# Kernel optimization log

Measured on AMD Instinct MI355X. Metric: run time of the kernel, lower is better.

Reference implementation:

```python
import jax, jax.numpy as jnp
import numpy as np
from jax import lax

TAU = 20.0
DT = 1.0
THRESH = 1.0

# Hard-threshold spike with surrogate gradient (triangular window around thresh),
# matching torch SpikeFunction.
@jax.custom_vjp
def spike(v):
    return (v >= THRESH).astype(v.dtype)

def _spike_fwd(v):
    return spike(v), v

def _spike_bwd(v, g):
    return (g * jnp.clip(1.0 - jnp.abs(v - THRESH), 0.0, 1.0),)

spike.defvjp(_spike_fwd, _spike_bwd)


def setup_inputs() -> dict:
    key = jax.random.key(0)
    B, F, T = 64, 2048, 512
    x = jax.random.normal(key, (B, F, T), dtype=jnp.float32)
    return {"x": x}


def reference(x) -> jnp.ndarray:
    # x: [B, F, T]; sequential LIF membrane scan over T with spike + hard reset.
    B, F, T = x.shape

    def step(v, x_t):
        v = v + (x_t - v) * (DT / TAU)
        s = spike(v)
        v = v * (1.0 - s)  # reset-to-zero on spike
        return v, s

    x_tmajor = jnp.moveaxis(x, 2, 0)  # [T, B, F]
    v0 = jnp.zeros((B, F), dtype=x.dtype)
    _, spikes = lax.scan(step, v0, x_tmajor)  # spikes: [T, B, F]
    return jnp.moveaxis(spikes, 0, 2)  # [B, F, T]
```

## Files before the change

### kernel.cpp

```cpp
#include <hip/hip_runtime.h>


typedef float f4 __attribute__((ext_vector_type(4)));

#define T_LEN 512
#define ROWS_PER_WAVE 16
#define WAVES_PER_BLOCK 4

__device__ __forceinline__ f4 shfl4(f4 v, int src) {
    f4 r;
    r[0] = __shfl(v[0], src, 64);
    r[1] = __shfl(v[1], src, 64);
    r[2] = __shfl(v[2], src, 64);
    r[3] = __shfl(v[3], src, 64);
    return r;
}

__global__ __launch_bounds__(256, 4)
void lif_kernel(const float* __restrict__ x, float* __restrict__ out) {
    constexpr float  K  = 1.0f / 20.0f;
    constexpr double Kd = (double)(1.0f / 20.0f);
    constexpr double A1 = 1.0 - Kd;
    constexpr double A2 = A1 * A1;
    constexpr double A4 = A2 * A2;
    constexpr double A8 = A4 * A4;
    constexpr double A16 = A8 * A8;
    constexpr double A32 = A16 * A16;
    constexpr double A64 = A32 * A32;
    constexpr double A128 = A64 * A64;
    constexpr double A256 = A128 * A128;
    constexpr float C[6] = {(float)A8,  (float)A16,  (float)A32,
                            (float)A64, (float)A128, (float)A256};

    const int lane = threadIdx.x & 63;
    const int wid  = blockIdx.x * WAVES_PER_BLOCK + (threadIdx.x >> 6);
    const size_t row0 = (size_t)wid * ROWS_PER_WAVE;

    const int s0 = (2 * lane) & 63;
    const int s1 = (2 * lane + 1) & 63;
    const bool lo = (lane < 32);

    const f4 zero4 = {0.f, 0.f, 0.f, 0.f};

    f4 A0, B0, A1v, B1v;
    {
        const float* p0 = x + row0 * T_LEN + lane * 4;
        A0  = __builtin_nontemporal_load((const f4*)p0);
        B0  = __builtin_nontemporal_load((const f4*)(p0 + 256));
        A1v = __builtin_nontemporal_load((const f4*)(p0 + T_LEN));
        B1v = __builtin_nontemporal_load((const f4*)(p0 + T_LEN + 256));
    }

#define STEP(RR, AV, BV)                                                      \
    {                                                                         \
        const size_t base = (row0 + (RR)) * (size_t)T_LEN;                    \
        float* ob = out + base + lane * 4;                                    \
                  \
        __builtin_nontemporal_store(zero4, (f4*)ob);                          \
        __builtin_nontemporal_store(zero4, (f4*)(ob + 256));                  \
               \
        const f4 ga = shfl4(AV, s0), gb = shfl4(AV, s1);                      \
        const f4 ha = shfl4(BV, s0), hb = shfl4(BV, s1);                      \
        const f4 q0 = lo ? ga : ha;                                           \
        const f4 q1 = lo ? gb : hb;                                           \
                  \
        if ((RR) + 2 < ROWS_PER_WAVE) {                                       \
            const float* pr = x + (row0 + (RR) + 2) * T_LEN + lane * 4;       \
            AV = __builtin_nontemporal_load((const f4*)pr);                   \
            BV = __builtin_nontemporal_load((const f4*)(pr + 256));           \
        }                                                                     \
                        \
        float b = 0.0f;                                                       \
        _Pragma("unroll")                                                     \
        for (int j = 0; j < 4; ++j) b = b + (q0[j] - b) * K;                  \
        _Pragma("unroll")                                                     \
        for (int j = 0; j < 4; ++j) b = b + (q1[j] - b) * K;                  \
                 \
        _Pragma("unroll")                                                     \
        for (int s = 0; s < 6; ++s) {                                         \
            const float o = __shfl_up(b, 1 << s);                             \
            const float f = fmaf(o, C[s], b);                                 \
            b = (lane >= (1 << s)) ? f : b;                                   \
        }                                                                     \
        float u = __shfl_up(b, 1);                                            \
        u = (lane == 0) ? 0.0f : u;                                           \
                      \
        float v = u;                                                          \
        float mx = -1.0f;                                                     \
        _Pragma("unroll")                                                     \
        for (int j = 0; j < 4; ++j) {                                         \
            v = v + (q0[j] - v) * K;                                          \
            mx = fmaxf(mx, v);                                                \
        }                                                                     \
        _Pragma("unroll")                                                     \
        for (int j = 0; j < 4; ++j) {                                         \
            v = v + (q1[j] - v) * K;                                          \
            mx = fmaxf(mx, v);                                                \
        }                                                                     \
        if (__builtin_expect(__ballot(mx >= 0.95f) != 0, 0)) {                \
                  \
            asm volatile("s_waitcnt vmcnt(0)" ::: "memory");                  \
            const float* xr = x + base;                                       \
            unsigned m = 0;                                                   \
            float vv = 0.0f;                                                  \
            for (int t = 0; t < T_LEN; ++t) {                                 \
                const float xt = xr[t];                                       \
                vv = vv + (xt - vv) * K;                                      \
                const bool fire = (vv >= 1.0f);                               \
                if (fire) vv = 0.0f;                                          \
                if (fire && ((t >> 3) == lane)) m |= (1u << (t & 7));         \
            }                                                                 \
            float* orow = out + base + (size_t)lane * 8;                      \
            while (m) {                                                       \
                const int j = __builtin_ctz(m);                               \
                m &= m - 1;                                                   \
                orow[j] = 1.0f;                                               \
            }                                                                 \
        }                                                                     \
    }

    STEP(0,  A0, B0)  STEP(1,  A1v, B1v)
    STEP(2,  A0, B0)  STEP(3,  A1v, B1v)
    STEP(4,  A0, B0)  STEP(5,  A1v, B1v)
    STEP(6,  A0, B0)  STEP(7,  A1v, B1v)
    STEP(8,  A0, B0)  STEP(9,  A1v, B1v)
    STEP(10, A0, B0)  STEP(11, A1v, B1v)
    STEP(12, A0, B0)  STEP(13, A1v, B1v)
    STEP(14, A0, B0)  STEP(15, A1v, B1v)
#undef STEP
}

extern "C" void kernel_launch(void* const* d_in, const int* in_sizes, int n_in,
                              void* d_out, int out_size, void* d_ws, size_t ws_size,
                              hipStream_t stream) {
    const float* x = (const float*)d_in[0];
    float* out = (float*)d_out;
    const int rows = in_sizes[0] / T_LEN;
    const int grid = rows / (ROWS_PER_WAVE * WAVES_PER_BLOCK);
    lif_kernel<<<dim3(grid), dim3(64 * WAVES_PER_BLOCK), 0, stream>>>(x, out);
}
```

Measured before the change: 417.3 us.

## Split zero-fill into separate kernel and scan halves without lane-remapping shuffles

Output zeroing moves out of the scan kernel into its own grid-stride fill kernel launched first. The scan kernel no longer shuffles loaded data to make each lane's eight elements contiguous. Instead it runs two chained 64-lane scans, one per half-row, and carries the first half's final value into the second, which removes about a third of the cross-lane shuffles per row. Rows per wave go from 16 to 32 and the row loop is now a runtime loop. The cost is a second kernel launch with a separate write pass, and no overlap between the output stores and the input reads.

```diff
diff --git a/kernel.cpp b/kernel.cpp
--- a/kernel.cpp
+++ b/kernel.cpp
@@ -4,43 +4,37 @@
 typedef float f4 __attribute__((ext_vector_type(4)));
 
 #define T_LEN 512
-#define ROWS_PER_WAVE 16
-#define WAVES_PER_BLOCK 4
+#define RPW 32
+#define WPB 4
 
-__device__ __forceinline__ f4 shfl4(f4 v, int src) {
-    f4 r;
-    r[0] = __shfl(v[0], src, 64);
-    r[1] = __shfl(v[1], src, 64);
-    r[2] = __shfl(v[2], src, 64);
-    r[3] = __shfl(v[3], src, 64);
-    return r;
+__global__ __launch_bounds__(256)
+void zfill_kernel(f4* __restrict__ out, int n4) {
+    const f4 z = {0.f, 0.f, 0.f, 0.f};
+    int i = blockIdx.x * 256 + threadIdx.x;
+    const int stride = gridDim.x * 256;
+    for (; i < n4; i += stride)
+        __builtin_nontemporal_store(z, out + i);
 }
 
 __global__ __launch_bounds__(256, 4)
-void lif_kernel(const float* __restrict__ x, float* __restrict__ out) {
-    constexpr float  K  = 1.0f / 20.0f;
-    constexpr double Kd = (double)(1.0f / 20.0f);
-    constexpr double A1 = 1.0 - Kd;
-    constexpr double A2 = A1 * A1;
-    constexpr double A4 = A2 * A2;
-    constexpr double A8 = A4 * A4;
-    constexpr double A16 = A8 * A8;
-    constexpr double A32 = A16 * A16;
-    constexpr double A64 = A32 * A32;
-    constexpr double A128 = A64 * A64;
-    constexpr double A256 = A128 * A128;
-    constexpr float C[6] = {(float)A8,  (float)A16,  (float)A32,
-                            (float)A64, (float)A128, (float)A256};
+void lif_scan_kernel(const float* __restrict__ x, float* __restrict__ out) {
+    constexpr float  K   = 1.0f / 20.0f;
+    constexpr double Kd  = (double)(1.0f / 20.0f);
+    constexpr double A1d = 1.0 - Kd;
+    constexpr double A2d = A1d * A1d;
+    constexpr double A4d = A2d * A2d;
+    constexpr double A8d = A4d * A4d;
+    constexpr double A16d = A8d * A8d;
+    constexpr double A32d = A16d * A16d;
+    constexpr double A64d = A32d * A32d;
+    constexpr double A128d = A64d * A64d;
+    constexpr float C4[6] = {(float)A4d,  (float)A8d,  (float)A16d,
+                             (float)A32d, (float)A64d, (float)A128d};
+    constexpr float A4f = (float)A4d;
 
     const int lane = threadIdx.x & 63;
-    const int wid  = blockIdx.x * WAVES_PER_BLOCK + (threadIdx.x >> 6);
-    const size_t row0 = (size_t)wid * ROWS_PER_WAVE;
-
-    const int s0 = (2 * lane) & 63;
-    const int s1 = (2 * lane + 1) & 63;
-    const bool lo = (lane < 32);
-
-    const f4 zero4 = {0.f, 0.f, 0.f, 0.f};
+    const int wid  = blockIdx.x * WPB + (threadIdx.x >> 6);
+    const size_t row0 = (size_t)wid * RPW;
 
     f4 A0, B0, A1v, B1v;
     {
@@ -54,79 +48,80 @@
 #define STEP(RR, AV, BV)                                                      \
     {                                                                         \
         const size_t base = (row0 + (RR)) * (size_t)T_LEN;                    \
-        float* ob = out + base + lane * 4;                                    \
-                  \
-        __builtin_nontemporal_store(zero4, (f4*)ob);                          \
-        __builtin_nontemporal_store(zero4, (f4*)(ob + 256));                  \
-               \
-        const f4 ga = shfl4(AV, s0), gb = shfl4(AV, s1);                      \
-        const f4 ha = shfl4(BV, s0), hb = shfl4(BV, s1);                      \
-        const f4 q0 = lo ? ga : ha;                                           \
-        const f4 q1 = lo ? gb : hb;                                           \
-                  \
-        if ((RR) + 2 < ROWS_PER_WAVE) {                                       \
-            const float* pr = x + (row0 + (RR) + 2) * T_LEN + lane * 4;       \
+        const f4 qa = AV, qb = BV;                                            \
+        if ((RR) + 2 < RPW) {      \
+            const float* pr = x + base + 2 * T_LEN + lane * 4;                \
             AV = __builtin_nontemporal_load((const f4*)pr);                   \
             BV = __builtin_nontemporal_load((const f4*)(pr + 256));           \
         }                                                                     \
-                        \
-        float b = 0.0f;                                                       \
+                                           \
+        float bA = 0.0f;                                                      \
         _Pragma("unroll")                                                     \
-        for (int j = 0; j < 4; ++j) b = b + (q0[j] - b) * K;                  \
-        _Pragma("unroll")                                                     \
-        for (int j = 0; j < 4; ++j) b = b + (q1[j] - b) * K;                  \
-                 \
+        for (int j = 0; j < 4; ++j) bA = bA + (qa[j] - bA) * K;               \
         _Pragma("unroll")                                                     \
         for (int s = 0; s < 6; ++s) {                                         \
-            const float o = __shfl_up(b, 1 << s);                             \
-            const float f = fmaf(o, C[s], b);                                 \
-            b = (lane >= (1 << s)) ? f : b;                                   \
+            const float o = __shfl_up(bA, 1 << s);                            \
+            const float f = fmaf(o, C4[s], bA);                               \
+            bA = (lane >= (1 << s)) ? f : bA;                                 \
         }                                                                     \
-        float u = __shfl_up(b, 1);                                            \
-        u = (lane == 0) ? 0.0f : u;                                           \
-                      \
-        float v = u;                                                          \
-        float mx = -1.0f;                                                     \
+        const float carry = __shfl(bA, 63);             \
+        float uA = __shfl_up(bA, 1);                                          \
+        uA = (lane == 0) ? 0.0f : uA;                                         \
+                \
+        float bB = 0.0f;                                                      \
+        _Pragma("unroll")                                                     \
+        for (int j = 0; j < 4; ++j) bB = bB + (qb[j] - bB) * K;               \
+        bB = (lane == 0) ? fmaf(carry, A4f, bB) : bB;                         \
+        _Pragma("unroll")                                                     \
+        for (int s = 0; s < 6; ++s) {                                         \
+            const float o = __shfl_up(bB, 1 << s);                            \
+            const float f = fmaf(o, C4[s], bB);                               \
+            bB = (lane >= (1 << s)) ? f : bB;                                 \
+        }                                                                     \
+        float uB = __shfl_up(bB, 1);                                          \
+        uB = (lane == 0) ? carry : uB;                                        \
+               \
+        float v = uA, mx = -1.0f;                                             \
         _Pragma("unroll")                                                     \
         for (int j = 0; j < 4; ++j) {                                         \
-            v = v + (q0[j] - v) * K;                                          \
+            v = v + (qa[j] - v) * K;                                          \
             mx = fmaxf(mx, v);                                                \
         }                                                                     \
+        v = uB;                                                               \
         _Pragma("unroll")                                                     \
         for (int j = 0; j < 4; ++j) {                                         \
-            v = v + (q1[j] - v) * K;                                          \
+            v = v + (qb[j] - v) * K;                                          \
             mx = fmaxf(mx, v);                                                \
         }                                                                     \
         if (__builtin_expect(__ballot(mx >= 0.95f) != 0, 0)) {                \
-                  \
-            asm volatile("s_waitcnt vmcnt(0)" ::: "memory");                  \
+                   \
             const float* xr = x + base;                                       \
             unsigned m = 0;                                                   \
             float vv = 0.0f;                                                  \
             for (int t = 0; t < T_LEN; ++t) {                                 \
-                const float xt = xr[t];                                       \
+                const float xt = xr[t];           \
                 vv = vv + (xt - vv) * K;                                      \
-                const bool fire = (vv >= 1.0f);                               \
-                if (fire) vv = 0.0f;                                          \
-                if (fire && ((t >> 3) == lane)) m |= (1u << (t & 7));         \
+                if (vv >= 1.0f) {                                             \
+                    vv = 0.0f;                                                \
+                    const int q = t >> 2;                                     \
+                    if (q == lane)      m |= 1u << (t & 3);                   \
+                    if (q == lane + 64) m |= 1u << ((t & 3) + 4);             \
+                }                                                             \
             }                                                                 \
-            float* orow = out + base + (size_t)lane * 8;                      \
-            while (m) {                                                       \
-                const int j = __builtin_ctz(m);                               \
-                m &= m - 1;                                                   \
-                orow[j] = 1.0f;                                               \
-            }                                                                 \
+            float* oA = out + base + (size_t)lane * 4;                        \
+            _Pragma("unroll")                                                 \
+            for (int j = 0; j < 4; ++j)                                       \
+                if ((m >> j) & 1u) oA[j] = 1.0f;                              \
+            _Pragma("unroll")                                                 \
+            for (int j = 0; j < 4; ++j)                                       \
+                if ((m >> (j + 4)) & 1u) oA[256 + j] = 1.0f;                  \
         }                                                                     \
     }
 
-    STEP(0,  A0, B0)  STEP(1,  A1v, B1v)
-    STEP(2,  A0, B0)  STEP(3,  A1v, B1v)
-    STEP(4,  A0, B0)  STEP(5,  A1v, B1v)
-    STEP(6,  A0, B0)  STEP(7,  A1v, B1v)
-    STEP(8,  A0, B0)  STEP(9,  A1v, B1v)
-    STEP(10, A0, B0)  STEP(11, A1v, B1v)
-    STEP(12, A0, B0)  STEP(13, A1v, B1v)
-    STEP(14, A0, B0)  STEP(15, A1v, B1v)
+    for (int rr = 0; rr < RPW; rr += 2) {
+        STEP(rr,     A0,  B0)
+        STEP(rr + 1, A1v, B1v)
+    }
 #undef STEP
 }
 
@@ -135,7 +130,10 @@
                               hipStream_t stream) {
     const float* x = (const float*)d_in[0];
     float* out = (float*)d_out;
+
+    zfill_kernel<<<dim3(2048), dim3(256), 0, stream>>>((f4*)out, out_size / 4);
+
     const int rows = in_sizes[0] / T_LEN;
-    const int grid = rows / (ROWS_PER_WAVE * WAVES_PER_BLOCK);
-    lif_kernel<<<dim3(grid), dim3(64 * WAVES_PER_BLOCK), 0, stream>>>(x, out);
+    const int grid = rows / (RPW * WPB);
+    lif_scan_kernel<<<dim3(grid), dim3(256), 0, stream>>>(x, out);
 }
```

Result: slower. 431.0 us (+3.3%).
